# Kernel tuning notes

Hardware: AMD Instinct MI355X
Metric: run time of the kernel (lower is better)

Reference implementation:

```python
import jax, jax.numpy as jnp
import numpy as np

B, N, H = 8, 2048, 256

def setup_inputs() -> dict:
    key = jax.random.key(0)
    k1, k2, k3, k4, k5 = jax.random.split(key, 5)
    h = jax.random.normal(k1, (B, N, H), dtype=jnp.float32)
    node_mask = jnp.ones((B, N, 1), dtype=jnp.float32)
    n_nodes = N  # unused by the forward math, kept for signature fidelity
    s1 = 1.0 / np.sqrt(H)
    W1 = jax.random.uniform(k2, (H, H), minval=-s1, maxval=s1, dtype=jnp.float32)
    b1 = jax.random.uniform(k3, (H,), minval=-s1, maxval=s1, dtype=jnp.float32)
    w2 = jax.random.uniform(k4, (H,), minval=-s1, maxval=s1, dtype=jnp.float32)
    b2 = jax.random.uniform(k5, (), minval=-s1, maxval=s1, dtype=jnp.float32)
    return {"h": h, "node_mask": node_mask, "n_nodes": n_nodes,
            "W1": W1, "b1": b1, "w2": w2, "b2": b2}

def reference(h, node_mask, n_nodes, W1, b1, w2, b2):
    # node_dec: Linear + SiLU
    x = jax.nn.silu(jnp.einsum('bnh,oh->bno', h, W1) + b1)  # [B,N,H]
    # pre_di applied to pairwise difference is linear, so factor:
    # pre_di(x_i - x_j) = (x_i @ w2) - (x_j @ w2) + b2
    s = jnp.einsum('bnh,h->bn', x, w2)                       # [B,N]
    out = s[:, :, None] - s[:, None, :] + b2                 # [B,N,N]
    return out.astype(jnp.int64)                             # torch .long() truncates
```

## Files before the change

kernel.cpp:

```cpp
#include <hip/hip_runtime.h>
#include <math.h>

#define B_ 8
#define N_ 2048
#define H_ 256

typedef double d4 __attribute__((ext_vector_type(4)));

__global__ __launch_bounds__(256)
void transpose_w1(const float* __restrict__ W1, float* __restrict__ W1T) {
    W1T[(size_t)blockIdx.x * H_ + threadIdx.x] =
        W1[(size_t)threadIdx.x * H_ + blockIdx.x];
}

__global__ __launch_bounds__(64)
void probe_kernel(double* __restrict__ pw) {
    const int l = threadIdx.x;
    d4 z = {0.0, 0.0, 0.0, 0.0};
    d4 r1 = __builtin_amdgcn_mfma_f64_16x16x4f64((double)(l + 1), 1.0, z, 0, 0, 0);
    d4 r2 = __builtin_amdgcn_mfma_f64_16x16x4f64(1.0, (double)(l + 1), z, 0, 0, 0);
    d4 r3 = __builtin_amdgcn_mfma_f64_16x16x4f64((double)(l & 15), 1.0, z, 0, 0, 0);
    if (l == 0)  { pw[0] = r1[0]; pw[1] = r2[0]; pw[5] = 7777.0; }
    if (l == 1)  { pw[2] = r3[0]; }
    if (l == 16) { pw[3] = r3[2]; pw[4] = r2[2]; }
}

__device__ __forceinline__ int layout_var(const double* pw) {
    if (pw[0] != 100.0 || pw[1] != 100.0) return 0;
    if (pw[2] == 0.0 && pw[3] == 24.0)  return 1;
    if (pw[2] == 0.0 && pw[3] == 36.0)  return 3;
    if (pw[2] == 4.0 && pw[4] == 124.0) return 2;
    if (pw[2] == 4.0 && pw[4] == 136.0) return 4;
    return 0;
}

__global__ __launch_bounds__(256)
__attribute__((amdgpu_waves_per_eu(2, 4)))
void s_mfma_uni(const float* __restrict__ hp, const float* __restrict__ W1T,
                const float* __restrict__ b1, const float* __restrict__ w2,
                double* __restrict__ s_out, const double* __restrict__ pw) {
    const int var = layout_var(pw);
    if (var == 0) return;
    __shared__ double spart[4][16];
    const int t = threadIdx.x;
    const int lane = t & 63;
    const int wave = __builtin_amdgcn_readfirstlane(t >> 6);
    const int a15 = lane & 15, g = lane >> 4;
    const int m0 = blockIdx.x * 16;
    const int oc = wave * 64;
    const float* ap = hp + (size_t)(m0 + a15) * H_ + g;
    const float* bp = W1T + (size_t)g * H_ + oc + a15;

    d4 acc[4];
    #pragma unroll
    for (int ot = 0; ot < 4; ++ot) acc[ot] = (d4){0.0, 0.0, 0.0, 0.0};

    float ac0, ac1, bc[8];
    ac0 = ap[0];
    ac1 = ap[4];
    #pragma unroll
    for (int ot = 0; ot < 4; ++ot) {
        bc[ot]     = bp[ot * 16];
        bc[4 + ot] = bp[4 * H_ + ot * 16];
    }

    for (int kc = 0; kc < H_; kc += 8) {
        const int kn = (kc + 8 < H_) ? (kc + 8) : 0;
        const float an0 = ap[kn];
        const float an1 = ap[kn + 4];
        float bn[8];
        #pragma unroll
        for (int ot = 0; ot < 4; ++ot) {
            bn[ot]     = bp[(size_t)kn * H_ + ot * 16];
            bn[4 + ot] = bp[(size_t)(kn + 4) * H_ + ot * 16];
        }
        const double av0 = (double)ac0;
        #pragma unroll
        for (int ot = 0; ot < 4; ++ot)
            acc[ot] = __builtin_amdgcn_mfma_f64_16x16x4f64(
                av0, (double)bc[ot], acc[ot], 0, 0, 0);
        const double av1 = (double)ac1;
        #pragma unroll
        for (int ot = 0; ot < 4; ++ot)
            acc[ot] = __builtin_amdgcn_mfma_f64_16x16x4f64(
                av1, (double)bc[4 + ot], acc[ot], 0, 0, 0);
        ac0 = an0; ac1 = an1;
        #pragma unroll
        for (int q = 0; q < 8; ++q) bc[q] = bn[q];
    }

    if (var == 1 || var == 3) {
        double psum[4] = {0.0, 0.0, 0.0, 0.0};
        #pragma unroll
        for (int ot = 0; ot < 4; ++ot) {
            const int o = oc + ot * 16 + a15;
            const double bb = (double)b1[o];
            const double ww = (double)w2[o];
            #pragma unroll
            for (int v = 0; v < 4; ++v) {
                const double u = acc[ot][v] + bb;
                psum[v] += ww * (u / (1.0 + exp(-u)));
            }
        }
        #pragma unroll
        for (int v = 0; v < 4; ++v) {
            double x = psum[v];
            x += __shfl_xor(x, 1, 64);
            x += __shfl_xor(x, 2, 64);
            x += __shfl_xor(x, 4, 64);
            x += __shfl_xor(x, 8, 64);
            psum[v] = x;
        }
        if (a15 == 0) {
            #pragma unroll
            for (int v = 0; v < 4; ++v) {
                const int row = (var == 1) ? (g * 4 + v) : (g + 4 * v);
                spart[wave][row] = psum[v];
            }
        }
    } else {
        double ps = 0.0;
        #pragma unroll
        for (int ot = 0; ot < 4; ++ot) {
            #pragma unroll
            for (int v = 0; v < 4; ++v) {
                const int cv = (var == 2) ? (4 * g + v) : (g + 4 * v);
                const int o = oc + ot * 16 + cv;
                const double u = acc[ot][v] + (double)b1[o];
                ps += (double)w2[o] * (u / (1.0 + exp(-u)));
            }
        }
        ps += __shfl_xor(ps, 16, 64);
        ps += __shfl_xor(ps, 32, 64);
        if (g == 0) spart[wave][a15] = ps;
    }
    __syncthreads();
    if (t < 16)
        s_out[m0 + t] = spart[0][t] + spart[1][t] + spart[2][t] + spart[3][t];
}

__global__ __launch_bounds__(256)
__attribute__((amdgpu_waves_per_eu(2, 4)))
void s_valu_kernel(const float* __restrict__ hp, const float* __restrict__ W1T,
                   const float* __restrict__ b1, const float* __restrict__ w2,
                   double* __restrict__ s_out, const double* __restrict__ pw) {
    if (layout_var(pw) != 0) return;
    const int t = threadIdx.x;
    const int lane = t & 63;
    const int wave = __builtin_amdgcn_readfirstlane(t >> 6);
    const int m0 = blockIdx.x * 16 + wave * 4;
    const int o0 = lane * 4;
    const float* hr = hp + (size_t)m0 * H_;
    const float* wp = W1T + o0;

    double acc[4][4];
    #pragma unroll
    for (int j = 0; j < 4; ++j)
        #pragma unroll
        for (int r = 0; r < 4; ++r) acc[j][r] = 0.0;

    float4 wA[8], wB[8];
    float hA[32], hB[32];

    #define LOADW(dst, kcv)                                                   \
        do {                                                                  \
            _Pragma("unroll")                                                 \
            for (int kk = 0; kk < 8; ++kk)                                    \
                dst[kk] = *reinterpret_cast<const float4*>(                   \
                    wp + (size_t)((kcv) + kk) * H_);                          \
        } while (0)

    #define LOADH(dst, kcv)                                                   \
        do {                                                                  \
            _Pragma("unroll")                                                 \
            for (int r = 0; r < 4; ++r)                                       \
                _Pragma("unroll")                                             \
                for (int kk = 0; kk < 8; ++kk)                                \
                    dst[r * 8 + kk] = hr[r * H_ + (kcv) + kk];                \
        } while (0)

    #define COMPUTE(wv, hbuf)                                                 \
        do {                                                                  \
            _Pragma("unroll")                                                 \
            for (int kk = 0; kk < 8; ++kk) {                                  \
                const double h0 = (double)hbuf[0 * 8 + kk];                   \
                const double h1 = (double)hbuf[1 * 8 + kk];                   \
                const double h2 = (double)hbuf[2 * 8 + kk];                   \
                const double h3 = (double)hbuf[3 * 8 + kk];                   \
                const double a0 = (double)wv[kk].x;                           \
                const double a1 = (double)wv[kk].y;                           \
                const double a2 = (double)wv[kk].z;                           \
                const double a3 = (double)wv[kk].w;                           \
                acc[0][0] = fma(a0, h0, acc[0][0]);                           \
                acc[0][1] = fma(a0, h1, acc[0][1]);                           \
                acc[0][2] = fma(a0, h2, acc[0][2]);                           \
                acc[0][3] = fma(a0, h3, acc[0][3]);                           \
                acc[1][0] = fma(a1, h0, acc[1][0]);                           \
                acc[1][1] = fma(a1, h1, acc[1][1]);                           \
                acc[1][2] = fma(a1, h2, acc[1][2]);                           \
                acc[1][3] = fma(a1, h3, acc[1][3]);                           \
                acc[2][0] = fma(a2, h0, acc[2][0]);                           \
                acc[2][1] = fma(a2, h1, acc[2][1]);                           \
                acc[2][2] = fma(a2, h2, acc[2][2]);                           \
                acc[2][3] = fma(a2, h3, acc[2][3]);                           \
                acc[3][0] = fma(a3, h0, acc[3][0]);                           \
                acc[3][1] = fma(a3, h1, acc[3][1]);                           \
                acc[3][2] = fma(a3, h2, acc[3][2]);                           \
                acc[3][3] = fma(a3, h3, acc[3][3]);                           \
            }                                                                 \
        } while (0)

    LOADW(wA, 0);
    LOADH(hA, 0);
    for (int kc = 0; kc < H_; kc += 16) {
        LOADW(wB, kc + 8);
        LOADH(hB, kc + 8);
        COMPUTE(wA, hA);
        if (kc + 16 < H_) {
            LOADW(wA, kc + 16);
            LOADH(hA, kc + 16);
        }
        COMPUTE(wB, hB);
    }
    #undef LOADW
    #undef LOADH
    #undef COMPUTE

    const float4 b1v = *reinterpret_cast<const float4*>(b1 + o0);
    const float4 w2v = *reinterpret_cast<const float4*>(w2 + o0);
    double psum[4] = {0.0, 0.0, 0.0, 0.0};
    #define EPI(j, bc, wc)                                                    \
        do {                                                                  \
            const double bb = (double)bc, ww = (double)wc;                    \
            _Pragma("unroll")                                                 \
            for (int r = 0; r < 4; ++r) {                                     \
                const double u = acc[j][r] + bb;                              \
                psum[r] += ww * (u / (1.0 + exp(-u)));                        \
            }                                                                 \
        } while (0)
    EPI(0, b1v.x, w2v.x);
    EPI(1, b1v.y, w2v.y);
    EPI(2, b1v.z, w2v.z);
    EPI(3, b1v.w, w2v.w);
    #undef EPI

    #pragma unroll
    for (int r = 0; r < 4; ++r) {
        double v = psum[r];
        v += __shfl_xor(v, 1, 64);
        v += __shfl_xor(v, 2, 64);
        v += __shfl_xor(v, 4, 64);
        v += __shfl_xor(v, 8, 64);
        v += __shfl_xor(v, 16, 64);
        v += __shfl_xor(v, 32, 64);
        if (lane == 0) s_out[m0 + r] = v;
    }
}

__global__ __launch_bounds__(256)
void pair_kernel(const double* __restrict__ s, const float* __restrict__ b2p,
                 int* __restrict__ out) {
    const double b2 = (double)b2p[0];
    const unsigned total4 = (unsigned)(B_) * (unsigned)(N_) * (unsigned)(N_) / 4u;
    const unsigned stride = gridDim.x * blockDim.x;
    for (unsigned idx = blockIdx.x * blockDim.x + threadIdx.x; idx < total4;
         idx += stride) {
        const unsigned base = idx * 4u;
        const unsigned bi  = base >> 22;
        const unsigned rem = base & ((1u << 22) - 1u);
        const unsigned i   = rem >> 11;
        const unsigned j   = rem & (N_ - 1u);
        const double si = s[bi * N_ + i];
        const double* sp = s + bi * N_ + j;
        const double sj0 = sp[0], sj1 = sp[1], sj2 = sp[2], sj3 = sp[3];
        int4 o;
        o.x = (int)trunc((si - sj0) + b2);
        o.y = (int)trunc((si - sj1) + b2);
        o.z = (int)trunc((si - sj2) + b2);
        o.w = (int)trunc((si - sj3) + b2);
        *reinterpret_cast<int4*>(out + base) = o;
    }
}

extern "C" void kernel_launch(void* const* d_in, const int* in_sizes, int n_in,
                              void* d_out, int out_size, void* d_ws, size_t ws_size,
                              hipStream_t stream) {
    const float* hp = (const float*)d_in[0];
    const float* W1 = (const float*)d_in[3];
    const float* b1 = (const float*)d_in[4];
    const float* w2 = (const float*)d_in[5];
    const float* b2 = (const float*)d_in[6];

    float*  W1T = (float*)d_ws;
    double* s   = (double*)((char*)d_ws + H_ * H_ * sizeof(float));
    double* pw  = (double*)((char*)d_ws + 384 * 1024);
    int* out = (int*)d_out;

    probe_kernel<<<1, 64, 0, stream>>>(pw);
    transpose_w1<<<H_, H_, 0, stream>>>(W1, W1T);
    s_mfma_uni<<<(B_ * N_) / 16, 256, 0, stream>>>(hp, W1T, b1, w2, s, pw);
    s_valu_kernel<<<(B_ * N_) / 16, 256, 0, stream>>>(hp, W1T, b1, w2, s, pw);
    pair_kernel<<<2048, 256, 0, stream>>>(s, b2, out);
}
```

Baseline: 81.52 us.

## Inline MFMA layout probe and process two row tiles per block

Removes the separate probe kernel launch: each wave now runs the three MFMA probe instructions itself and broadcasts the results with shuffles, so no global probe buffer is read. The MFMA projection kernel now handles 32 rows per block, using two 16-row M tiles that share each loaded W1T fragment. This halves the grid and the B-operand loads per row. It doubles accumulator registers and adds redundant probe MFMAs in every wave, which may cut occupancy and leaves fewer blocks to spread across CUs.

```diff
diff --git a/kernel.cpp b/kernel.cpp
--- a/kernel.cpp
+++ b/kernel.cpp
@@ -13,24 +13,22 @@
         W1[(size_t)threadIdx.x * H_ + blockIdx.x];
 }
 
-__global__ __launch_bounds__(64)
-void probe_kernel(double* __restrict__ pw) {
-    const int l = threadIdx.x;
+__device__ __forceinline__ int self_probe_var() {
+    const int l = threadIdx.x & 63;
     d4 z = {0.0, 0.0, 0.0, 0.0};
     d4 r1 = __builtin_amdgcn_mfma_f64_16x16x4f64((double)(l + 1), 1.0, z, 0, 0, 0);
     d4 r2 = __builtin_amdgcn_mfma_f64_16x16x4f64(1.0, (double)(l + 1), z, 0, 0, 0);
     d4 r3 = __builtin_amdgcn_mfma_f64_16x16x4f64((double)(l & 15), 1.0, z, 0, 0, 0);
-    if (l == 0)  { pw[0] = r1[0]; pw[1] = r2[0]; pw[5] = 7777.0; }
-    if (l == 1)  { pw[2] = r3[0]; }
-    if (l == 16) { pw[3] = r3[2]; pw[4] = r2[2]; }
-}
-
-__device__ __forceinline__ int layout_var(const double* pw) {
-    if (pw[0] != 100.0 || pw[1] != 100.0) return 0;
-    if (pw[2] == 0.0 && pw[3] == 24.0)  return 1;
-    if (pw[2] == 0.0 && pw[3] == 36.0)  return 3;
-    if (pw[2] == 4.0 && pw[4] == 124.0) return 2;
-    if (pw[2] == 4.0 && pw[4] == 136.0) return 4;
+    const double pw0 = __shfl(r1[0], 0, 64);
+    const double pw1 = __shfl(r2[0], 0, 64);
+    const double pw2 = __shfl(r3[0], 1, 64);
+    const double pw3 = __shfl(r3[2], 16, 64);
+    const double pw4 = __shfl(r2[2], 16, 64);
+    if (pw0 != 100.0 || pw1 != 100.0) return 0;
+    if (pw2 == 0.0 && pw3 == 24.0)  return 1;
+    if (pw2 == 0.0 && pw3 == 36.0)  return 3;
+    if (pw2 == 4.0 && pw4 == 124.0) return 2;
+    if (pw2 == 4.0 && pw4 == 136.0) return 4;
     return 0;
 }
 
@@ -38,104 +36,135 @@
 __attribute__((amdgpu_waves_per_eu(2, 4)))
 void s_mfma_uni(const float* __restrict__ hp, const float* __restrict__ W1T,
                 const float* __restrict__ b1, const float* __restrict__ w2,
-                double* __restrict__ s_out, const double* __restrict__ pw) {
-    const int var = layout_var(pw);
+                double* __restrict__ s_out) {
+    const int var = self_probe_var();
     if (var == 0) return;
-    __shared__ double spart[4][16];
+    __shared__ double spart[4][32];
     const int t = threadIdx.x;
     const int lane = t & 63;
     const int wave = __builtin_amdgcn_readfirstlane(t >> 6);
     const int a15 = lane & 15, g = lane >> 4;
-    const int m0 = blockIdx.x * 16;
+    const int m0 = blockIdx.x * 32;
     const int oc = wave * 64;
-    const float* ap = hp + (size_t)(m0 + a15) * H_ + g;
-    const float* bp = W1T + (size_t)g * H_ + oc + a15;
-
-    d4 acc[4];
+    const float* ap0 = hp + (size_t)(m0 + a15) * H_ + g;
+    const float* ap1 = hp + (size_t)(m0 + 16 + a15) * H_ + g;
+    const float* bp  = W1T + (size_t)g * H_ + oc + a15;
+
+    d4 acc[2][4];
     #pragma unroll
-    for (int ot = 0; ot < 4; ++ot) acc[ot] = (d4){0.0, 0.0, 0.0, 0.0};
-
-    float ac0, ac1, bc[8];
-    ac0 = ap[0];
-    ac1 = ap[4];
+    for (int mt = 0; mt < 2; ++mt)
+        #pragma unroll
+        for (int ot = 0; ot < 4; ++ot) acc[mt][ot] = (d4){0.0, 0.0, 0.0, 0.0};
+
+    float ac[4], an[4];
+    float bcv[8], bnv[8];
+    ac[0] = ap0[0]; ac[1] = ap0[4]; ac[2] = ap1[0]; ac[3] = ap1[4];
     #pragma unroll
     for (int ot = 0; ot < 4; ++ot) {
-        bc[ot]     = bp[ot * 16];
-        bc[4 + ot] = bp[4 * H_ + ot * 16];
+        bcv[ot]     = bp[ot * 16];
+        bcv[4 + ot] = bp[4 * H_ + ot * 16];
     }
 
     for (int kc = 0; kc < H_; kc += 8) {
         const int kn = (kc + 8 < H_) ? (kc + 8) : 0;
-        const float an0 = ap[kn];
-        const float an1 = ap[kn + 4];
-        float bn[8];
+        an[0] = ap0[kn]; an[1] = ap0[kn + 4];
+        an[2] = ap1[kn]; an[3] = ap1[kn + 4];
         #pragma unroll
         for (int ot = 0; ot < 4; ++ot) {
-            bn[ot]     = bp[(size_t)kn * H_ + ot * 16];
-            bn[4 + ot] = bp[(size_t)(kn + 4) * H_ + ot * 16];
-        }
-        const double av0 = (double)ac0;
-        #pragma unroll
-        for (int ot = 0; ot < 4; ++ot)
-            acc[ot] = __builtin_amdgcn_mfma_f64_16x16x4f64(
-                av0, (double)bc[ot], acc[ot], 0, 0, 0);
-        const double av1 = (double)ac1;
-        #pragma unroll
-        for (int ot = 0; ot < 4; ++ot)
-            acc[ot] = __builtin_amdgcn_mfma_f64_16x16x4f64(
-                av1, (double)bc[4 + ot], acc[ot], 0, 0, 0);
-        ac0 = an0; ac1 = an1;
-        #pragma unroll
-        for (int q = 0; q < 8; ++q) bc[q] = bn[q];
+            bnv[ot]     = bp[(size_t)kn * H_ + ot * 16];
+            bnv[4 + ot] = bp[(size_t)(kn + 4) * H_ + ot * 16];
+        }
+        {
+            const double a0 = (double)ac[0], a1 = (double)ac[2];
+            #pragma unroll
+            for (int ot = 0; ot < 4; ++ot) {
+                const double bv = (double)bcv[ot];
+                acc[0][ot] = __builtin_amdgcn_mfma_f64_16x16x4f64(a0, bv, acc[0][ot], 0, 0, 0);
+                acc[1][ot] = __builtin_amdgcn_mfma_f64_16x16x4f64(a1, bv, acc[1][ot], 0, 0, 0);
+            }
+        }
+        {
+            const double a0 = (double)ac[1], a1 = (double)ac[3];
+            #pragma unroll
+            for (int ot = 0; ot < 4; ++ot) {
+                const double bv = (double)bcv[4 + ot];
+                acc[0][ot] = __builtin_amdgcn_mfma_f64_16x16x4f64(a0, bv, acc[0][ot], 0, 0, 0);
+                acc[1][ot] = __builtin_amdgcn_mfma_f64_16x16x4f64(a1, bv, acc[1][ot], 0, 0, 0);
+            }
+        }
+        #pragma unroll
+        for (int q = 0; q < 4; ++q) ac[q] = an[q];
+        #pragma unroll
+        for (int q = 0; q < 8; ++q) bcv[q] = bnv[q];
     }
 
     if (var == 1 || var == 3) {
-        double psum[4] = {0.0, 0.0, 0.0, 0.0};
+        double psum[2][4];
+        #pragma unroll
+        for (int mt = 0; mt < 2; ++mt)
+            #pragma unroll
+            for (int v = 0; v < 4; ++v) psum[mt][v] = 0.0;
         #pragma unroll
         for (int ot = 0; ot < 4; ++ot) {
             const int o = oc + ot * 16 + a15;
             const double bb = (double)b1[o];
             const double ww = (double)w2[o];
             #pragma unroll
+            for (int mt = 0; mt < 2; ++mt)
+                #pragma unroll
+                for (int v = 0; v < 4; ++v) {
+                    const double u = acc[mt][ot][v] + bb;
+                    psum[mt][v] += ww * (u / (1.0 + exp(-u)));
+                }
+        }
+        #pragma unroll
+        for (int mt = 0; mt < 2; ++mt)
+            #pragma unroll
             for (int v = 0; v < 4; ++v) {
-                const double u = acc[ot][v] + bb;
-                psum[v] += ww * (u / (1.0 + exp(-u)));
+                double x = psum[mt][v];
+                x += __shfl_xor(x, 1, 64);
+                x += __shfl_xor(x, 2, 64);
+                x += __shfl_xor(x, 4, 64);
+                x += __shfl_xor(x, 8, 64);
+                psum[mt][v] = x;
             }
-        }
-        #pragma unroll
-        for (int v = 0; v < 4; ++v) {
-            double x = psum[v];
-            x += __shfl_xor(x, 1, 64);
-            x += __shfl_xor(x, 2, 64);
-            x += __shfl_xor(x, 4, 64);
-            x += __shfl_xor(x, 8, 64);
-            psum[v] = x;
-        }
         if (a15 == 0) {
             #pragma unroll
-            for (int v = 0; v < 4; ++v) {
-                const int row = (var == 1) ? (g * 4 + v) : (g + 4 * v);
-                spart[wave][row] = psum[v];
-            }
+            for (int mt = 0; mt < 2; ++mt)
+                #pragma unroll
+                for (int v = 0; v < 4; ++v) {
+                    const int row = (var == 1) ? (4 * g + v) : (g + 4 * v);
+                    spart[wave][mt * 16 + row] = psum[mt][v];
+                }
         }
     } else {
-        double ps = 0.0;
-        #pragma unroll
-        for (int ot = 0; ot < 4; ++ot) {
+        double ps[2] = {0.0, 0.0};
+        #pragma unroll
+        for (int ot = 0; ot < 4; ++ot)
             #pragma unroll
             for (int v = 0; v < 4; ++v) {
                 const int cv = (var == 2) ? (4 * g + v) : (g + 4 * v);
                 const int o = oc + ot * 16 + cv;
-                const double u = acc[ot][v] + (double)b1[o];
-                ps += (double)w2[o] * (u / (1.0 + exp(-u)));
+                const double bb = (double)b1[o];
+                const double ww = (double)w2[o];
+                #pragma unroll
+                for (int mt = 0; mt < 2; ++mt) {
+                    const double u = acc[mt][ot][v] + bb;
+                    ps[mt] += ww * (u / (1.0 + exp(-u)));
+                }
             }
-        }
-        ps += __shfl_xor(ps, 16, 64);
-        ps += __shfl_xor(ps, 32, 64);
-        if (g == 0) spart[wave][a15] = ps;
+        #pragma unroll
+        for (int mt = 0; mt < 2; ++mt) {
+            ps[mt] += __shfl_xor(ps[mt], 16, 64);
+            ps[mt] += __shfl_xor(ps[mt], 32, 64);
+        }
+        if (g == 0) {
+            spart[wave][a15]      = ps[0];
+            spart[wave][16 + a15] = ps[1];
+        }
     }
     __syncthreads();
-    if (t < 16)
+    if (t < 32)
         s_out[m0 + t] = spart[0][t] + spart[1][t] + spart[2][t] + spart[3][t];
 }
 
@@ -143,8 +172,8 @@
 __attribute__((amdgpu_waves_per_eu(2, 4)))
 void s_valu_kernel(const float* __restrict__ hp, const float* __restrict__ W1T,
                    const float* __restrict__ b1, const float* __restrict__ w2,
-                   double* __restrict__ s_out, const double* __restrict__ pw) {
-    if (layout_var(pw) != 0) return;
+                   double* __restrict__ s_out) {
+    if (self_probe_var() != 0) return;
     const int t = threadIdx.x;
     const int lane = t & 63;
     const int wave = __builtin_amdgcn_readfirstlane(t >> 6);
@@ -293,12 +322,10 @@
 
     float*  W1T = (float*)d_ws;
     double* s   = (double*)((char*)d_ws + H_ * H_ * sizeof(float));
-    double* pw  = (double*)((char*)d_ws + 384 * 1024);
     int* out = (int*)d_out;
 
-    probe_kernel<<<1, 64, 0, stream>>>(pw);
     transpose_w1<<<H_, H_, 0, stream>>>(W1, W1T);
-    s_mfma_uni<<<(B_ * N_) / 16, 256, 0, stream>>>(hp, W1T, b1, w2, s, pw);
-    s_valu_kernel<<<(B_ * N_) / 16, 256, 0, stream>>>(hp, W1T, b1, w2, s, pw);
+    s_mfma_uni<<<(B_ * N_) / 32, 256, 0, stream>>>(hp, W1T, b1, w2, s);
+    s_valu_kernel<<<(B_ * N_) / 16, 256, 0, stream>>>(hp, W1T, b1, w2, s);
     pair_kernel<<<2048, 256, 0, stream>>>(s, b2, out);
 }
```

Measured after the change: 74.62 us. -8.5%, faster.

## Pack W1 for vectorized MFMA B loads and probe MFMA layout in-kernel

Applied to the files above, without the earlier changes.

Adds a pack kernel that reorders W1 so each lane can fetch its B operands for four output tiles as contiguous float4 loads. The MFMA k-loop is restructured around 16-element chunks with double-buffered prefetch, instead of scalar strided loads from the transposed weights. The separate probe kernel and its global-memory handshake are replaced by an in-kernel MFMA probe using shuffles, which removes one launch at the cost of repeating the probe in every block. One extra launch (pack_w1) is added, and transpose_w1 still runs for the VALU fallback.

```diff
diff --git a/kernel.cpp b/kernel.cpp
--- a/kernel.cpp
+++ b/kernel.cpp
@@ -13,33 +13,37 @@
         W1[(size_t)threadIdx.x * H_ + blockIdx.x];
 }
 
-__global__ __launch_bounds__(64)
-void probe_kernel(double* __restrict__ pw) {
-    const int l = threadIdx.x;
+__global__ __launch_bounds__(256)
+void pack_w1(const float* __restrict__ W1, float* __restrict__ W1P) {
+    const int o = blockIdx.x, k = threadIdx.x;
+    W1P[(size_t)o * H_ + (k & 3) * 64 + (k >> 2)] = W1[(size_t)o * H_ + k];
+}
+
+__device__ __forceinline__ int self_probe_var() {
+    const int l = threadIdx.x & 63;
     d4 z = {0.0, 0.0, 0.0, 0.0};
     d4 r1 = __builtin_amdgcn_mfma_f64_16x16x4f64((double)(l + 1), 1.0, z, 0, 0, 0);
     d4 r2 = __builtin_amdgcn_mfma_f64_16x16x4f64(1.0, (double)(l + 1), z, 0, 0, 0);
     d4 r3 = __builtin_amdgcn_mfma_f64_16x16x4f64((double)(l & 15), 1.0, z, 0, 0, 0);
-    if (l == 0)  { pw[0] = r1[0]; pw[1] = r2[0]; pw[5] = 7777.0; }
-    if (l == 1)  { pw[2] = r3[0]; }
-    if (l == 16) { pw[3] = r3[2]; pw[4] = r2[2]; }
-}
-
-__device__ __forceinline__ int layout_var(const double* pw) {
-    if (pw[0] != 100.0 || pw[1] != 100.0) return 0;
-    if (pw[2] == 0.0 && pw[3] == 24.0)  return 1;
-    if (pw[2] == 0.0 && pw[3] == 36.0)  return 3;
-    if (pw[2] == 4.0 && pw[4] == 124.0) return 2;
-    if (pw[2] == 4.0 && pw[4] == 136.0) return 4;
+    const double pw0 = __shfl(r1[0], 0, 64);
+    const double pw1 = __shfl(r2[0], 0, 64);
+    const double pw2 = __shfl(r3[0], 1, 64);
+    const double pw3 = __shfl(r3[2], 16, 64);
+    const double pw4 = __shfl(r2[2], 16, 64);
+    if (pw0 != 100.0 || pw1 != 100.0) return 0;
+    if (pw2 == 0.0 && pw3 == 24.0)  return 1;
+    if (pw2 == 0.0 && pw3 == 36.0)  return 3;
+    if (pw2 == 4.0 && pw4 == 124.0) return 2;
+    if (pw2 == 4.0 && pw4 == 136.0) return 4;
     return 0;
 }
 
 __global__ __launch_bounds__(256)
 __attribute__((amdgpu_waves_per_eu(2, 4)))
-void s_mfma_uni(const float* __restrict__ hp, const float* __restrict__ W1T,
+void s_mfma_uni(const float* __restrict__ hp, const float* __restrict__ W1P,
                 const float* __restrict__ b1, const float* __restrict__ w2,
-                double* __restrict__ s_out, const double* __restrict__ pw) {
-    const int var = layout_var(pw);
+                double* __restrict__ s_out) {
+    const int var = self_probe_var();
     if (var == 0) return;
     __shared__ double spart[4][16];
     const int t = threadIdx.x;
@@ -49,45 +53,57 @@
     const int m0 = blockIdx.x * 16;
     const int oc = wave * 64;
     const float* ap = hp + (size_t)(m0 + a15) * H_ + g;
-    const float* bp = W1T + (size_t)g * H_ + oc + a15;
+    const float* bq0 = W1P + ((size_t)(oc + 0 * 16 + a15) * 4 + g) * 64;
+    const float* bq1 = W1P + ((size_t)(oc + 1 * 16 + a15) * 4 + g) * 64;
+    const float* bq2 = W1P + ((size_t)(oc + 2 * 16 + a15) * 4 + g) * 64;
+    const float* bq3 = W1P + ((size_t)(oc + 3 * 16 + a15) * 4 + g) * 64;
 
     d4 acc[4];
     #pragma unroll
     for (int ot = 0; ot < 4; ++ot) acc[ot] = (d4){0.0, 0.0, 0.0, 0.0};
 
-    float ac0, ac1, bc[8];
-    ac0 = ap[0];
-    ac1 = ap[4];
-    #pragma unroll
-    for (int ot = 0; ot < 4; ++ot) {
-        bc[ot]     = bp[ot * 16];
-        bc[4 + ot] = bp[4 * H_ + ot * 16];
-    }
-
-    for (int kc = 0; kc < H_; kc += 8) {
-        const int kn = (kc + 8 < H_) ? (kc + 8) : 0;
-        const float an0 = ap[kn];
-        const float an1 = ap[kn + 4];
-        float bn[8];
-        #pragma unroll
-        for (int ot = 0; ot < 4; ++ot) {
-            bn[ot]     = bp[(size_t)kn * H_ + ot * 16];
-            bn[4 + ot] = bp[(size_t)(kn + 4) * H_ + ot * 16];
-        }
-        const double av0 = (double)ac0;
-        #pragma unroll
-        for (int ot = 0; ot < 4; ++ot)
-            acc[ot] = __builtin_amdgcn_mfma_f64_16x16x4f64(
-                av0, (double)bc[ot], acc[ot], 0, 0, 0);
-        const double av1 = (double)ac1;
-        #pragma unroll
-        for (int ot = 0; ot < 4; ++ot)
-            acc[ot] = __builtin_amdgcn_mfma_f64_16x16x4f64(
-                av1, (double)bc[4 + ot], acc[ot], 0, 0, 0);
-        ac0 = an0; ac1 = an1;
-        #pragma unroll
-        for (int q = 0; q < 8; ++q) bc[q] = bn[q];
-    }
+    float bc[16], bn[16];
+    float ac[4], an[4];
+
+    #define LOADB(dst, c)                                                     \
+        do {                                                                  \
+            float4 f0 = *reinterpret_cast<const float4*>(bq0 + (c) * 4);      \
+            float4 f1 = *reinterpret_cast<const float4*>(bq1 + (c) * 4);      \
+            float4 f2 = *reinterpret_cast<const float4*>(bq2 + (c) * 4);      \
+            float4 f3 = *reinterpret_cast<const float4*>(bq3 + (c) * 4);      \
+            dst[0]=f0.x;  dst[1]=f0.y;  dst[2]=f0.z;  dst[3]=f0.w;            \
+            dst[4]=f1.x;  dst[5]=f1.y;  dst[6]=f1.z;  dst[7]=f1.w;            \
+            dst[8]=f2.x;  dst[9]=f2.y;  dst[10]=f2.z; dst[11]=f2.w;           \
+            dst[12]=f3.x; dst[13]=f3.y; dst[14]=f3.z; dst[15]=f3.w;           \
+        } while (0)
+
+    #define LOADA(dst, c)                                                     \
+        do {                                                                  \
+            _Pragma("unroll")                                                 \
+            for (int q = 0; q < 4; ++q) dst[q] = ap[(c) * 16 + q * 4];        \
+        } while (0)
+
+    LOADB(bc, 0);
+    LOADA(ac, 0);
+    for (int c = 0; c < 16; ++c) {
+        const int cn = (c + 1 < 16) ? (c + 1) : 0;
+        LOADB(bn, cn);
+        LOADA(an, cn);
+        #pragma unroll
+        for (int q = 0; q < 4; ++q) {
+            const double av = (double)ac[q];
+            acc[0] = __builtin_amdgcn_mfma_f64_16x16x4f64(av, (double)bc[0 * 4 + q], acc[0], 0, 0, 0);
+            acc[1] = __builtin_amdgcn_mfma_f64_16x16x4f64(av, (double)bc[1 * 4 + q], acc[1], 0, 0, 0);
+            acc[2] = __builtin_amdgcn_mfma_f64_16x16x4f64(av, (double)bc[2 * 4 + q], acc[2], 0, 0, 0);
+            acc[3] = __builtin_amdgcn_mfma_f64_16x16x4f64(av, (double)bc[3 * 4 + q], acc[3], 0, 0, 0);
+        }
+        #pragma unroll
+        for (int q = 0; q < 4; ++q) ac[q] = an[q];
+        #pragma unroll
+        for (int q = 0; q < 16; ++q) bc[q] = bn[q];
+    }
+    #undef LOADB
+    #undef LOADA
 
     if (var == 1 || var == 3) {
         double psum[4] = {0.0, 0.0, 0.0, 0.0};
@@ -114,14 +130,14 @@
         if (a15 == 0) {
             #pragma unroll
             for (int v = 0; v < 4; ++v) {
-                const int row = (var == 1) ? (g * 4 + v) : (g + 4 * v);
+                const int row = (var == 1) ? (4 * g + v) : (g + 4 * v);
                 spart[wave][row] = psum[v];
             }
         }
     } else {
         double ps = 0.0;
         #pragma unroll
-        for (int ot = 0; ot < 4; ++ot) {
+        for (int ot = 0; ot < 4; ++ot)
             #pragma unroll
             for (int v = 0; v < 4; ++v) {
                 const int cv = (var == 2) ? (4 * g + v) : (g + 4 * v);
@@ -129,7 +145,6 @@
                 const double u = acc[ot][v] + (double)b1[o];
                 ps += (double)w2[o] * (u / (1.0 + exp(-u)));
             }
-        }
         ps += __shfl_xor(ps, 16, 64);
         ps += __shfl_xor(ps, 32, 64);
         if (g == 0) spart[wave][a15] = ps;
@@ -143,8 +158,8 @@
 __attribute__((amdgpu_waves_per_eu(2, 4)))
 void s_valu_kernel(const float* __restrict__ hp, const float* __restrict__ W1T,
                    const float* __restrict__ b1, const float* __restrict__ w2,
-                   double* __restrict__ s_out, const double* __restrict__ pw) {
-    if (layout_var(pw) != 0) return;
+                   double* __restrict__ s_out) {
+    if (self_probe_var() != 0) return;
     const int t = threadIdx.x;
     const int lane = t & 63;
     const int wave = __builtin_amdgcn_readfirstlane(t >> 6);
@@ -292,13 +307,13 @@
     const float* b2 = (const float*)d_in[6];
 
     float*  W1T = (float*)d_ws;
-    double* s   = (double*)((char*)d_ws + H_ * H_ * sizeof(float));
-    double* pw  = (double*)((char*)d_ws + 384 * 1024);
+    float*  W1P = (float*)((char*)d_ws + 256 * 1024);
+    double* s   = (double*)((char*)d_ws + 512 * 1024);
     int* out = (int*)d_out;
 
-    probe_kernel<<<1, 64, 0, stream>>>(pw);
     transpose_w1<<<H_, H_, 0, stream>>>(W1, W1T);
-    s_mfma_uni<<<(B_ * N_) / 16, 256, 0, stream>>>(hp, W1T, b1, w2, s, pw);
-    s_valu_kernel<<<(B_ * N_) / 16, 256, 0, stream>>>(hp, W1T, b1, w2, s, pw);
+    pack_w1<<<H_, H_, 0, stream>>>(W1, W1P);
+    s_mfma_uni<<<(B_ * N_) / 16, 256, 0, stream>>>(hp, W1P, b1, w2, s);
+    s_valu_kernel<<<(B_ * N_) / 16, 256, 0, stream>>>(hp, W1T, b1, w2, s);
     pair_kernel<<<2048, 256, 0, stream>>>(s, b2, out);
 }
```

Result: slower. 110.0 us (+34.9%).
